# Performance work log

Hardware: AMD Instinct MI355X
Metric: run time of the kernel (lower is better)

Reference implementation:

```python
import jax, jax.numpy as jnp
import numpy as np

N, E, H, L, G = 50000, 800000, 128, 4, 64

def setup_inputs() -> dict:
    key = jax.random.key(0)
    ks = jax.random.split(key, 16)
    s = 0.05
    x = jax.random.normal(ks[0], (N, H), jnp.float32)
    edge_index = jax.random.randint(ks[1], (2, E), 0, N)
    edge_attr = jax.random.normal(ks[2], (E, 1), jnp.float32)
    # sorted graph assignment covering all G graphs (batch[-1]+1 == G)
    batch = (jnp.arange(N) * G) // N
    conv_W1 = jax.random.normal(ks[3], (L, H, H), jnp.float32) * s
    conv_b1 = jnp.zeros((L, H), jnp.float32)
    conv_W2 = jax.random.normal(ks[4], (L, H, H), jnp.float32) * s
    conv_b2 = jnp.zeros((L, H), jnp.float32)
    conv_eps = jnp.zeros((L,), jnp.float32)  # torch init: eps = 0
    edge_W = jax.random.normal(ks[5], (L, 1, H), jnp.float32) * s
    edge_b = jnp.zeros((L, H), jnp.float32)
    vn_W1 = jax.random.normal(ks[6], (L - 1, H, H), jnp.float32) * s
    vn_b1 = jnp.zeros((L - 1, H), jnp.float32)
    vn_W2 = jax.random.normal(ks[7], (L - 1, H, H), jnp.float32) * s
    vn_b2 = jnp.zeros((L - 1, H), jnp.float32)
    vn_emb = jnp.zeros((H,), jnp.float32)  # torch init: constant 0
    return dict(x=x, edge_attr=edge_attr, conv_W1=conv_W1, conv_b1=conv_b1,
                conv_W2=conv_W2, conv_b2=conv_b2, conv_eps=conv_eps,
                edge_W=edge_W, edge_b=edge_b, vn_W1=vn_W1, vn_b1=vn_b1,
                vn_W2=vn_W2, vn_b2=vn_b2, vn_emb=vn_emb,
                edge_index=edge_index, batch=batch)


def reference(x, edge_attr, conv_W1, conv_b1, conv_W2, conv_b2, conv_eps,
              edge_W, edge_b, vn_W1, vn_b1, vn_W2, vn_b2, vn_emb,
              edge_index, batch):
    src, tgt = edge_index[0], edge_index[1]
    # PyG mean aggregation: divide scatter-sum by in-degree (clamped to 1)
    deg = jnp.maximum(
        jax.ops.segment_sum(jnp.ones((E,), x.dtype), tgt, num_segments=N), 1.0)[:, None]
    vn = jnp.broadcast_to(vn_emb[None, :], (G, H))  # virtual node per graph
    h = x
    hs = []
    for i in range(L):
        h = h + vn[batch]
        edge_emb = edge_attr @ edge_W[i] + edge_b[i]          # [E,H]
        msg = jax.nn.relu(h[src] + edge_emb)                   # gather + relu
        agg = jax.ops.segment_sum(msg, tgt, num_segments=N) / deg  # mean scatter
        z = (1.0 + conv_eps[i]) * h + agg
        h = jax.nn.relu(z @ conv_W1[i] + conv_b1[i]) @ conv_W2[i] + conv_b2[i]
        hs.append(h)
        if i < L - 1:
            vt = jax.ops.segment_sum(hs[i], batch, num_segments=G) + vn
            vn = jax.nn.relu(
                jax.nn.relu(vt @ vn_W1[i] + vn_b1[i]) @ vn_W2[i] + vn_b2[i])
            # eval mode: dropout is identity
    return jnp.concatenate(hs, axis=1)  # [N, L*H] jumping-knowledge concat
```

## Files before the change

### kernel.cpp

```cpp
#include <hip/hip_runtime.h>

#define NN 50000
#define EE 800000
#define HH 128
#define LL 4
#define GG 64
#define NR 50048

typedef short bf16x8 __attribute__((ext_vector_type(8)));
typedef float f32x4 __attribute__((ext_vector_type(4)));

__device__ __forceinline__ unsigned bf_round(float f) {
  unsigned u = __float_as_uint(f);
  return (u + 0x7fffu + ((u >> 16) & 1u)) >> 16;
}
__device__ __forceinline__ unsigned bf_pack2(float lo, float hi) {
  return bf_round(lo) | (bf_round(hi) << 16);
}

__global__ __launch_bounds__(256) void count_kernel(const int* __restrict__ tgt,
                                                    int* __restrict__ cnt, int E) {
  int e = blockIdx.x * 256 + threadIdx.x;
  if (e < E) atomicAdd(&cnt[tgt[e]], 1);
}

__global__ __launch_bounds__(256) void blocksum_kernel(const int* __restrict__ cnt,
                                                       int* __restrict__ bs, int N) {
  int i = blockIdx.x * 256 + threadIdx.x;
  int v = (i < N) ? cnt[i] : 0;
  __shared__ int sm[256];
  sm[threadIdx.x] = v;
  __syncthreads();
  for (int s = 128; s >= 1; s >>= 1) {
    if (threadIdx.x < s) sm[threadIdx.x] += sm[threadIdx.x + s];
    __syncthreads();
  }
  if (threadIdx.x == 0) bs[blockIdx.x] = sm[0];
}

__global__ __launch_bounds__(256) void bs_scan_kernel(int* __restrict__ bs, int nb) {
  __shared__ int sm[256];
  int t = threadIdx.x;
  int v = (t < nb) ? bs[t] : 0;
  sm[t] = v;
  __syncthreads();
  for (int off = 1; off < 256; off <<= 1) {
    int u = (t >= off) ? sm[t - off] : 0;
    __syncthreads();
    sm[t] += u;
    __syncthreads();
  }
  if (t < nb) bs[t] = sm[t] - v;
  if (t == 255) bs[nb] = sm[255];
}

__global__ __launch_bounds__(256) void blockscan_kernel(const int* __restrict__ cnt,
                                                        const int* __restrict__ bs,
                                                        int* __restrict__ rp,
                                                        int* __restrict__ cur, int N, int nb) {
  int b = blockIdx.x, t = threadIdx.x;
  int i = b * 256 + t;
  int v = (i < N) ? cnt[i] : 0;
  __shared__ int sm[256];
  sm[t] = v;
  __syncthreads();
  for (int off = 1; off < 256; off <<= 1) {
    int u = (t >= off) ? sm[t - off] : 0;
    __syncthreads();
    sm[t] += u;
    __syncthreads();
  }
  if (i < N) { rp[i] = sm[t] - v + bs[b]; cur[i] = 0; }
  if (b == 0 && t == 0) rp[N] = bs[nb];
}

__global__ __launch_bounds__(256) void scatter_kernel(const int* __restrict__ src,
                                                      const int* __restrict__ tgt,
                                                      const float* __restrict__ attr,
                                                      const int* __restrict__ rp,
                                                      int* __restrict__ cur,
                                                      int2* __restrict__ es, int E) {
  int e = blockIdx.x * 256 + threadIdx.x;
  if (e < E) {
    int t = tgt[e];
    int p = rp[t] + atomicAdd(&cur[t], 1);
    int2 rec;
    rec.x = src[e];
    rec.y = __float_as_int(attr[e]);
    es[p] = rec;
  }
}

__global__ __launch_bounds__(256) void init_kernel(const float* __restrict__ W1,
                                                   const float* __restrict__ W2,
                                                   const float* __restrict__ emb,
                                                   short* __restrict__ wt1,
                                                   short* __restrict__ wt2,
                                                   float* __restrict__ vn,
                                                   float* __restrict__ part) {
  int idx = blockIdx.x * 256 + threadIdx.x;
  const int NW = 2 * LL * HH * HH;
  if (idx < NW) {
    int m = idx >> 14;
    int r = idx & 16383;
    int n = r >> 7, k = r & 127;
    const float* W = (m < LL) ? (W1 + (size_t)m * 16384) : (W2 + (size_t)(m - LL) * 16384);
    short* D = (m < LL) ? (wt1 + (size_t)m * 16384) : (wt2 + (size_t)(m - LL) * 16384);
    D[n * 128 + k] = (short)bf_round(W[k * 128 + n]);
  } else if (idx < NW + GG * HH) {
    int i = idx - NW;
    vn[i] = emb[i & (HH - 1)];
  } else if (idx < NW + 2 * GG * HH) {
    part[idx - NW - GG * HH] = 0.f;
  }
}

__global__ __launch_bounds__(256) void pack_kernel(const float4* __restrict__ hp, int pitch4,
                                                   const float4* __restrict__ vn,
                                                   const int* __restrict__ batch,
                                                   uint2* __restrict__ hbf, int N) {
  int idx = blockIdx.x * 256 + threadIdx.x;
  if (idx >= N * (HH / 4)) return;
  int n = idx >> 5;
  int c4 = idx & 31;
  int g = batch[n];
  float4 a = hp[(size_t)n * pitch4 + c4];
  float4 b = vn[g * 32 + c4];
  uint2 o;
  o.x = bf_pack2(a.x + b.x, a.y + b.y);
  o.y = bf_pack2(a.z + b.z, a.w + b.w);
  hbf[idx] = o;
}

__device__ __forceinline__ void accum8(float* acc, uint4 p, float a,
                                       const float4& ew0, const float4& ew1,
                                       const float4& eb0, const float4& eb1, float m) {
  float lo, hi;
  lo = __uint_as_float(p.x << 16); hi = __uint_as_float(p.x & 0xffff0000u);
  acc[0] += m * fmaxf(lo + fmaf(a, ew0.x, eb0.x), 0.f);
  acc[1] += m * fmaxf(hi + fmaf(a, ew0.y, eb0.y), 0.f);
  lo = __uint_as_float(p.y << 16); hi = __uint_as_float(p.y & 0xffff0000u);
  acc[2] += m * fmaxf(lo + fmaf(a, ew0.z, eb0.z), 0.f);
  acc[3] += m * fmaxf(hi + fmaf(a, ew0.w, eb0.w), 0.f);
  lo = __uint_as_float(p.z << 16); hi = __uint_as_float(p.z & 0xffff0000u);
  acc[4] += m * fmaxf(lo + fmaf(a, ew1.x, eb1.x), 0.f);
  acc[5] += m * fmaxf(hi + fmaf(a, ew1.y, eb1.y), 0.f);
  lo = __uint_as_float(p.w << 16); hi = __uint_as_float(p.w & 0xffff0000u);
  acc[6] += m * fmaxf(lo + fmaf(a, ew1.z, eb1.z), 0.f);
  acc[7] += m * fmaxf(hi + fmaf(a, ew1.w, eb1.w), 0.f);
}

__global__ __launch_bounds__(128) void agg_kernel(const uint4* __restrict__ hbf4,
                                                  const float* __restrict__ hp, int pitch,
                                                  const float* __restrict__ vnp,
                                                  const int* __restrict__ batch,
                                                  const int2* __restrict__ es,
                                                  const int* __restrict__ rp,
                                                  const float* __restrict__ eW,
                                                  const float* __restrict__ eb,
                                                  const float* __restrict__ epsp,
                                                  uint4* __restrict__ zb4, int N) {
  int wave = threadIdx.x >> 6;
  int lane = threadIdx.x & 63;
  int n = blockIdx.x * 2 + wave;
  if (n >= N) return;
  int q = lane >> 4;
  int c = lane & 15;
  float4 ew0 = *(const float4*)(eW + c * 8);
  float4 ew1 = *(const float4*)(eW + c * 8 + 4);
  float4 eb0 = *(const float4*)(eb + c * 8);
  float4 eb1 = *(const float4*)(eb + c * 8 + 4);
  int rs = rp[n], re = rp[n + 1];
  float acc[8];
#pragma unroll
  for (int j = 0; j < 8; ++j) acc[j] = 0.f;
  int k = rs;
  for (; k + 8 <= re; k += 8) {
    int2 e0 = es[k + q];
    int2 e1 = es[k + 4 + q];
    uint4 p0 = hbf4[(size_t)e0.x * 16 + c];
    uint4 p1 = hbf4[(size_t)e1.x * 16 + c];
    accum8(acc, p0, __int_as_float(e0.y), ew0, ew1, eb0, eb1, 1.f);
    accum8(acc, p1, __int_as_float(e1.y), ew0, ew1, eb0, eb1, 1.f);
  }
  for (; k < re; k += 4) {
    int idx = min(k + q, re - 1);
    int2 e = es[idx];
    float m = (k + q < re) ? 1.f : 0.f;
    uint4 p = hbf4[(size_t)e.x * 16 + c];
    accum8(acc, p, __int_as_float(e.y), ew0, ew1, eb0, eb1, m);
  }
#pragma unroll
  for (int j = 0; j < 8; ++j) {
    acc[j] += __shfl_xor(acc[j], 16);
    acc[j] += __shfl_xor(acc[j], 32);
  }
  int g = batch[n];
  const float* hrow = hp + (size_t)n * pitch + c * 8;
  const float* vrow = vnp + g * HH + c * 8;
  float4 h0 = *(const float4*)(hrow);
  float4 h1 = *(const float4*)(hrow + 4);
  float4 v0 = *(const float4*)(vrow);
  float4 v1 = *(const float4*)(vrow + 4);
  float inv = 1.f / fmaxf((float)(re - rs), 1.f);
  float onep = 1.f + epsp[0];
  uint4 o;
  o.x = bf_pack2(fmaf(onep, h0.x + v0.x, acc[0] * inv),
                 fmaf(onep, h0.y + v0.y, acc[1] * inv));
  o.y = bf_pack2(fmaf(onep, h0.z + v0.z, acc[2] * inv),
                 fmaf(onep, h0.w + v0.w, acc[3] * inv));
  o.z = bf_pack2(fmaf(onep, h1.x + v1.x, acc[4] * inv),
                 fmaf(onep, h1.y + v1.y, acc[5] * inv));
  o.w = bf_pack2(fmaf(onep, h1.z + v1.z, acc[6] * inv),
                 fmaf(onep, h1.w + v1.w, acc[7] * inv));
  if (q == 0) zb4[(size_t)n * 16 + c] = o;
}

__global__ __launch_bounds__(256) void mlp_kernel(const unsigned* __restrict__ zb,
                                                  const short* __restrict__ wt1,
                                                  const float* __restrict__ b1,
                                                  const short* __restrict__ wt2,
                                                  const float* __restrict__ b2,
                                                  float* __restrict__ out,
                                                  float* __restrict__ part,
                                                  int do_gs, int layer, int N) {
  __shared__ char smem[64 * 272];
  int tid = threadIdx.x;
  int w = tid >> 6, lane = tid & 63;
  int l15 = lane & 15, q = lane >> 4;
  int row0 = blockIdx.x * 64;
  int wrow = w * 16;

  const uint4* z4 = (const uint4*)zb;
#pragma unroll
  for (int it = 0; it < 4; ++it) {
    int f = lane + it * 64;
    int r = f >> 4, c16 = f & 15;
    uint4 v = z4[(size_t)(row0 + wrow + r) * 16 + c16];
    *(uint4*)(&smem[(wrow + r) * 272 + c16 * 16]) = v;
  }

  f32x4 zero = {0.f, 0.f, 0.f, 0.f};
  f32x4 acc[8];
#pragma unroll
  for (int j = 0; j < 8; ++j) acc[j] = zero;

#pragma unroll
  for (int s = 0; s < 4; ++s) {
    bf16x8 af = *(const bf16x8*)(&smem[(wrow + l15) * 272 + (s * 32 + q * 8) * 2]);
#pragma unroll
    for (int j = 0; j < 8; ++j) {
      bf16x8 bf = *(const bf16x8*)(wt1 + (size_t)(j * 16 + l15) * 128 + s * 32 + q * 8);
      acc[j] = __builtin_amdgcn_mfma_f32_16x16x32_bf16(af, bf, acc[j], 0, 0, 0);
    }
  }
#pragma unroll
  for (int j = 0; j < 8; ++j) {
    float bv = b1[j * 16 + l15];
#pragma unroll
    for (int r = 0; r < 4; ++r) {
      float v = fmaxf(acc[j][r] + bv, 0.f);
      *(short*)(&smem[(wrow + q * 4 + r) * 272 + (j * 16 + l15) * 2]) = (short)bf_round(v);
    }
    acc[j] = zero;
  }
#pragma unroll
  for (int s = 0; s < 4; ++s) {
    bf16x8 af = *(const bf16x8*)(&smem[(wrow + l15) * 272 + (s * 32 + q * 8) * 2]);
#pragma unroll
    for (int j = 0; j < 8; ++j) {
      bf16x8 bf = *(const bf16x8*)(wt2 + (size_t)(j * 16 + l15) * 128 + s * 32 + q * 8);
      acc[j] = __builtin_amdgcn_mfma_f32_16x16x32_bf16(af, bf, acc[j], 0, 0, 0);
    }
  }
  int g0 = (int)(((long long)row0 * GG) / NN);
#pragma unroll
  for (int j = 0; j < 8; ++j) {
    float bv = b2[j * 16 + l15];
    float s0 = 0.f, s1 = 0.f;
#pragma unroll
    for (int r = 0; r < 4; ++r) {
      int row = row0 + wrow + q * 4 + r;
      if (row < N) {
        float v = acc[j][r] + bv;
        out[(size_t)row * (LL * HH) + layer * HH + j * 16 + l15] = v;
        if (do_gs) {
          int rel = (int)(((long long)row * GG) / NN) - g0;
          if (rel == 0) s0 += v; else s1 += v;
        }
      }
    }
    if (do_gs) {
      s0 += __shfl_xor(s0, 16); s0 += __shfl_xor(s0, 32);
      s1 += __shfl_xor(s1, 16); s1 += __shfl_xor(s1, 32);
      if (q == 0) {
        atomicAdd(&part[g0 * HH + j * 16 + l15], s0);
        if (s1 != 0.f) atomicAdd(&part[(g0 + 1) * HH + j * 16 + l15], s1);
      }
    }
  }
}

__global__ __launch_bounds__(128) void vn_fused_kernel(float* __restrict__ part,
                                                       const float* __restrict__ W1,
                                                       const float* __restrict__ b1,
                                                       const float* __restrict__ W2,
                                                       const float* __restrict__ b2,
                                                       float* __restrict__ vn, int G) {
  int g = blockIdx.x, j = threadIdx.x;
  __shared__ float vr[128];
  __shared__ float tr[128];
  vr[j] = vn[g * HH + j] + part[g * HH + j];
  part[g * HH + j] = 0.f;
  __syncthreads();
  float a = b1[j];
  for (int k = 0; k < 128; ++k) a = fmaf(vr[k], W1[k * HH + j], a);
  tr[j] = fmaxf(a, 0.f);
  __syncthreads();
  float o = b2[j];
  for (int k = 0; k < 128; ++k) o = fmaf(tr[k], W2[k * HH + j], o);
  vn[g * HH + j] = fmaxf(o, 0.f);
}

extern "C" void kernel_launch(void* const* d_in, const int* in_sizes, int n_in,
                              void* d_out, int out_size, void* d_ws, size_t ws_size,
                              hipStream_t stream) {
  const int N = NN, E = EE, H = HH, L = LL, G = GG;
  const float* x          = (const float*)d_in[0];
  const float* edge_attr  = (const float*)d_in[1];
  const float* conv_W1    = (const float*)d_in[2];
  const float* conv_b1    = (const float*)d_in[3];
  const float* conv_W2    = (const float*)d_in[4];
  const float* conv_b2    = (const float*)d_in[5];
  const float* conv_eps   = (const float*)d_in[6];
  const float* edge_W     = (const float*)d_in[7];
  const float* edge_b     = (const float*)d_in[8];
  const float* vn_W1      = (const float*)d_in[9];
  const float* vn_b1      = (const float*)d_in[10];
  const float* vn_W2      = (const float*)d_in[11];
  const float* vn_b2      = (const float*)d_in[12];
  const float* vn_emb     = (const float*)d_in[13];
  const int*   edge_index = (const int*)d_in[14];
  const int*   batch      = (const int*)d_in[15];
  float* out = (float*)d_out;

  const int nb = (N + 255) / 256;

  char* ws = (char*)d_ws;
  size_t off = 0;
  auto take = [&](size_t bytes) -> void* {
    void* p = ws + off;
    off = (off + bytes + 255) & ~(size_t)255;
    return p;
  };
  int*      cnt  = (int*)take((size_t)N * 4);
  int*      cur  = (int*)take((size_t)N * 4);
  int*      rp   = (int*)take((size_t)(N + 1) * 4);
  int*      bs   = (int*)take((size_t)(nb + 1) * 4);
  int2*     es   = (int2*)take((size_t)E * 8);
  unsigned* hbf  = (unsigned*)take((size_t)N * (H / 2) * 4);
  unsigned* zb   = (unsigned*)take((size_t)NR * (H / 2) * 4);
  short*    wt1  = (short*)take((size_t)L * H * H * 2);
  short*    wt2  = (short*)take((size_t)L * H * H * 2);
  float*    part = (float*)take((size_t)G * H * 4);
  float*    vn   = (float*)take((size_t)G * H * 4);

  const int* src = edge_index;
  const int* tgt = edge_index + E;

  hipMemsetAsync(cnt, 0, (size_t)N * 4, stream);
  count_kernel<<<(E + 255) / 256, 256, 0, stream>>>(tgt, cnt, E);
  blocksum_kernel<<<nb, 256, 0, stream>>>(cnt, bs, N);
  bs_scan_kernel<<<1, 256, 0, stream>>>(bs, nb);
  blockscan_kernel<<<nb, 256, 0, stream>>>(cnt, bs, rp, cur, N, nb);
  scatter_kernel<<<(E + 255) / 256, 256, 0, stream>>>(src, tgt, edge_attr, rp, cur, es, E);
  init_kernel<<<(2 * L * H * H + 2 * G * H + 255) / 256, 256, 0, stream>>>(
      conv_W1, conv_W2, vn_emb, wt1, wt2, vn, part);

  for (int i = 0; i < L; ++i) {
    const float* hp;
    int pitch;
    if (i == 0) { hp = x; pitch = H; }
    else        { hp = out + (size_t)(i - 1) * H; pitch = L * H; }
    pack_kernel<<<(N * (H / 4) + 255) / 256, 256, 0, stream>>>(
        (const float4*)hp, pitch / 4, (const float4*)vn, batch, (uint2*)hbf, N);
    agg_kernel<<<(N + 1) / 2, 128, 0, stream>>>(
        (const uint4*)hbf, hp, pitch, vn, batch, es, rp,
        edge_W + (size_t)i * H, edge_b + (size_t)i * H,
        conv_eps + i, (uint4*)zb, N);
    mlp_kernel<<<NR / 64, 256, 0, stream>>>(
        zb, wt1 + (size_t)i * H * H, conv_b1 + (size_t)i * H,
        wt2 + (size_t)i * H * H, conv_b2 + (size_t)i * H, out, part,
        (i < L - 1) ? 1 : 0, i, N);
    if (i < L - 1) {
      vn_fused_kernel<<<G, 128, 0, stream>>>(part, vn_W1 + (size_t)i * H * H,
                                             vn_b1 + (size_t)i * H,
                                             vn_W2 + (size_t)i * H * H,
                                             vn_b2 + (size_t)i * H, vn, G);
    }
  }
}
```

Before: 620.5 us.

## Split aggregation into four column passes and fold edge bias into packed features

Result: slower. 825.6 us (+33.0%).

```diff
diff --git a/kernel.cpp b/kernel.cpp
--- a/kernel.cpp
+++ b/kernel.cpp
@@ -6,6 +6,7 @@
 #define LL 4
 #define GG 64
 #define NR 50048
+#define NBN 12500
 
 typedef short bf16x8 __attribute__((ext_vector_type(8)));
 typedef float f32x4 __attribute__((ext_vector_type(4)));
@@ -117,6 +118,7 @@
 
 __global__ __launch_bounds__(256) void pack_kernel(const float4* __restrict__ hp, int pitch4,
                                                    const float4* __restrict__ vn,
+                                                   const float4* __restrict__ ebias,
                                                    const int* __restrict__ batch,
                                                    uint2* __restrict__ hbf, int N) {
   int idx = blockIdx.x * 256 + threadIdx.x;
@@ -126,94 +128,85 @@
   int g = batch[n];
   float4 a = hp[(size_t)n * pitch4 + c4];
   float4 b = vn[g * 32 + c4];
+  float4 e = ebias[c4];
   uint2 o;
-  o.x = bf_pack2(a.x + b.x, a.y + b.y);
-  o.y = bf_pack2(a.z + b.z, a.w + b.w);
+  o.x = bf_pack2(a.x + b.x + e.x, a.y + b.y + e.y);
+  o.y = bf_pack2(a.z + b.z + e.z, a.w + b.w + e.w);
   hbf[idx] = o;
 }
 
-__device__ __forceinline__ void accum8(float* acc, uint4 p, float a,
-                                       const float4& ew0, const float4& ew1,
-                                       const float4& eb0, const float4& eb1, float m) {
-  float lo, hi;
-  lo = __uint_as_float(p.x << 16); hi = __uint_as_float(p.x & 0xffff0000u);
-  acc[0] += m * fmaxf(lo + fmaf(a, ew0.x, eb0.x), 0.f);
-  acc[1] += m * fmaxf(hi + fmaf(a, ew0.y, eb0.y), 0.f);
-  lo = __uint_as_float(p.y << 16); hi = __uint_as_float(p.y & 0xffff0000u);
-  acc[2] += m * fmaxf(lo + fmaf(a, ew0.z, eb0.z), 0.f);
-  acc[3] += m * fmaxf(hi + fmaf(a, ew0.w, eb0.w), 0.f);
-  lo = __uint_as_float(p.z << 16); hi = __uint_as_float(p.z & 0xffff0000u);
-  acc[4] += m * fmaxf(lo + fmaf(a, ew1.x, eb1.x), 0.f);
-  acc[5] += m * fmaxf(hi + fmaf(a, ew1.y, eb1.y), 0.f);
-  lo = __uint_as_float(p.w << 16); hi = __uint_as_float(p.w & 0xffff0000u);
-  acc[6] += m * fmaxf(lo + fmaf(a, ew1.z, eb1.z), 0.f);
-  acc[7] += m * fmaxf(hi + fmaf(a, ew1.w, eb1.w), 0.f);
-}
-
-__global__ __launch_bounds__(128) void agg_kernel(const uint4* __restrict__ hbf4,
+__device__ __forceinline__ void accum8s(float* acc, uint4 p, float a, float m,
+                                        const float4& ew0, const float4& ew1) {
+  acc[0] = fmaf(m, fmaxf(fmaf(a, ew0.x, __uint_as_float(p.x << 16)), 0.f), acc[0]);
+  acc[1] = fmaf(m, fmaxf(fmaf(a, ew0.y, __uint_as_float(p.x & 0xffff0000u)), 0.f), acc[1]);
+  acc[2] = fmaf(m, fmaxf(fmaf(a, ew0.z, __uint_as_float(p.y << 16)), 0.f), acc[2]);
+  acc[3] = fmaf(m, fmaxf(fmaf(a, ew0.w, __uint_as_float(p.y & 0xffff0000u)), 0.f), acc[3]);
+  acc[4] = fmaf(m, fmaxf(fmaf(a, ew1.x, __uint_as_float(p.z << 16)), 0.f), acc[4]);
+  acc[5] = fmaf(m, fmaxf(fmaf(a, ew1.y, __uint_as_float(p.z & 0xffff0000u)), 0.f), acc[5]);
+  acc[6] = fmaf(m, fmaxf(fmaf(a, ew1.z, __uint_as_float(p.w << 16)), 0.f), acc[6]);
+  acc[7] = fmaf(m, fmaxf(fmaf(a, ew1.w, __uint_as_float(p.w & 0xffff0000u)), 0.f), acc[7]);
+}
+
+__global__ __launch_bounds__(256) void agg_kernel(const uint4* __restrict__ hbf4,
                                                   const float* __restrict__ hp, int pitch,
                                                   const float* __restrict__ vnp,
                                                   const int* __restrict__ batch,
                                                   const int2* __restrict__ es,
                                                   const int* __restrict__ rp,
                                                   const float* __restrict__ eW,
-                                                  const float* __restrict__ eb,
                                                   const float* __restrict__ epsp,
                                                   uint4* __restrict__ zb4, int N) {
   int wave = threadIdx.x >> 6;
   int lane = threadIdx.x & 63;
-  int n = blockIdx.x * 2 + wave;
+  int pass = blockIdx.x / NBN;
+  int nb = blockIdx.x - pass * NBN;
+  int n = nb * 4 + wave;
   if (n >= N) return;
-  int q = lane >> 4;
-  int c = lane & 15;
-  float4 ew0 = *(const float4*)(eW + c * 8);
-  float4 ew1 = *(const float4*)(eW + c * 8 + 4);
-  float4 eb0 = *(const float4*)(eb + c * 8);
-  float4 eb1 = *(const float4*)(eb + c * 8 + 4);
+  int e = lane >> 2;
+  int c = lane & 3;
+  int col0 = pass * 32 + c * 8;
+  float4 ew0 = *(const float4*)(eW + col0);
+  float4 ew1 = *(const float4*)(eW + col0 + 4);
   int rs = rp[n], re = rp[n + 1];
+  int cnt = re - rs;
   float acc[8];
 #pragma unroll
   for (int j = 0; j < 8; ++j) acc[j] = 0.f;
-  int k = rs;
-  for (; k + 8 <= re; k += 8) {
-    int2 e0 = es[k + q];
-    int2 e1 = es[k + 4 + q];
-    uint4 p0 = hbf4[(size_t)e0.x * 16 + c];
-    uint4 p1 = hbf4[(size_t)e1.x * 16 + c];
-    accum8(acc, p0, __int_as_float(e0.y), ew0, ew1, eb0, eb1, 1.f);
-    accum8(acc, p1, __int_as_float(e1.y), ew0, ew1, eb0, eb1, 1.f);
-  }
-  for (; k < re; k += 4) {
-    int idx = min(k + q, re - 1);
-    int2 e = es[idx];
-    float m = (k + q < re) ? 1.f : 0.f;
-    uint4 p = hbf4[(size_t)e.x * 16 + c];
-    accum8(acc, p, __int_as_float(e.y), ew0, ew1, eb0, eb1, m);
+  for (int k = 0; k < cnt; k += 16) {
+    int idx = rs + min(k + e, cnt - 1);
+    int2 ed = es[idx];
+    float m = (k + e < cnt) ? 1.f : 0.f;
+    uint4 p = hbf4[(size_t)ed.x * 16 + pass * 4 + c];
+    accum8s(acc, p, __int_as_float(ed.y), m, ew0, ew1);
   }
 #pragma unroll
   for (int j = 0; j < 8; ++j) {
+    acc[j] += __shfl_xor(acc[j], 4);
+    acc[j] += __shfl_xor(acc[j], 8);
     acc[j] += __shfl_xor(acc[j], 16);
     acc[j] += __shfl_xor(acc[j], 32);
   }
-  int g = batch[n];
-  const float* hrow = hp + (size_t)n * pitch + c * 8;
-  const float* vrow = vnp + g * HH + c * 8;
-  float4 h0 = *(const float4*)(hrow);
-  float4 h1 = *(const float4*)(hrow + 4);
-  float4 v0 = *(const float4*)(vrow);
-  float4 v1 = *(const float4*)(vrow + 4);
-  float inv = 1.f / fmaxf((float)(re - rs), 1.f);
-  float onep = 1.f + epsp[0];
-  uint4 o;
-  o.x = bf_pack2(fmaf(onep, h0.x + v0.x, acc[0] * inv),
-                 fmaf(onep, h0.y + v0.y, acc[1] * inv));
-  o.y = bf_pack2(fmaf(onep, h0.z + v0.z, acc[2] * inv),
-                 fmaf(onep, h0.w + v0.w, acc[3] * inv));
-  o.z = bf_pack2(fmaf(onep, h1.x + v1.x, acc[4] * inv),
-                 fmaf(onep, h1.y + v1.y, acc[5] * inv));
-  o.w = bf_pack2(fmaf(onep, h1.z + v1.z, acc[6] * inv),
-                 fmaf(onep, h1.w + v1.w, acc[7] * inv));
-  if (q == 0) zb4[(size_t)n * 16 + c] = o;
+  if (e == 0) {
+    int g = batch[n];
+    const float* hrow = hp + (size_t)n * pitch + col0;
+    const float* vrow = vnp + g * HH + col0;
+    float4 h0 = *(const float4*)(hrow);
+    float4 h1 = *(const float4*)(hrow + 4);
+    float4 v0 = *(const float4*)(vrow);
+    float4 v1 = *(const float4*)(vrow + 4);
+    float inv = 1.f / fmaxf((float)cnt, 1.f);
+    float onep = 1.f + epsp[0];
+    uint4 o;
+    o.x = bf_pack2(fmaf(onep, h0.x + v0.x, acc[0] * inv),
+                   fmaf(onep, h0.y + v0.y, acc[1] * inv));
+    o.y = bf_pack2(fmaf(onep, h0.z + v0.z, acc[2] * inv),
+                   fmaf(onep, h0.w + v0.w, acc[3] * inv));
+    o.z = bf_pack2(fmaf(onep, h1.x + v1.x, acc[4] * inv),
+                   fmaf(onep, h1.y + v1.y, acc[5] * inv));
+    o.w = bf_pack2(fmaf(onep, h1.z + v1.z, acc[6] * inv),
+                   fmaf(onep, h1.w + v1.w, acc[7] * inv));
+    zb4[(size_t)n * 16 + pass * 4 + c] = o;
+  }
 }
 
 __global__ __launch_bounds__(256) void mlp_kernel(const unsigned* __restrict__ zb,
@@ -383,11 +376,11 @@
     if (i == 0) { hp = x; pitch = H; }
     else        { hp = out + (size_t)(i - 1) * H; pitch = L * H; }
     pack_kernel<<<(N * (H / 4) + 255) / 256, 256, 0, stream>>>(
-        (const float4*)hp, pitch / 4, (const float4*)vn, batch, (uint2*)hbf, N);
-    agg_kernel<<<(N + 1) / 2, 128, 0, stream>>>(
+        (const float4*)hp, pitch / 4, (const float4*)vn,
+        (const float4*)(edge_b + (size_t)i * H), batch, (uint2*)hbf, N);
+    agg_kernel<<<4 * NBN, 256, 0, stream>>>(
         (const uint4*)hbf, hp, pitch, vn, batch, es, rp,
-        edge_W + (size_t)i * H, edge_b + (size_t)i * H,
-        conv_eps + i, (uint4*)zb, N);
+        edge_W + (size_t)i * H, conv_eps + i, (uint4*)zb, N);
     mlp_kernel<<<NR / 64, 256, 0, stream>>>(
         zb, wt1 + (size_t)i * H * H, conv_b1 + (size_t)i * H,
         wt2 + (size_t)i * H * H, conv_b2 + (size_t)i * H, out, part,
```
